# Performance work log

Hardware: AMD Instinct MI355X
Metric: run time of the kernel (lower is better)

The kernel has to match this reference:

```python
import jax, jax.numpy as jnp
import numpy as np

N = 20000      # nodes
E = 640000     # edges
Z = 10         # elements (one-hot node_attrs dim)
H = 128        # hidden channels
B = 32         # graphs in batch
NB = 8         # Bessel basis size
L = 2          # interaction layers
R_MAX = 5.0


def _sph(u):
    # real spherical harmonics, lmax=2 -> 9 components; u: [E,3] unit vectors
    x, y, z = u[:, 0], u[:, 1], u[:, 2]
    c1 = 0.4886025119
    return jnp.stack([
        jnp.full_like(x, 0.2820947918),
        c1 * y, c1 * z, c1 * x,
        1.0925484306 * x * y,
        1.0925484306 * y * z,
        0.3153915653 * (3.0 * z * z - 1.0),
        1.0925484306 * x * z,
        0.5462742153 * (x * x - y * y),
    ], axis=-1)  # [E,9]


def _radial(r):
    # Bessel radial basis with smooth cosine cutoff; r: [E]
    n = jnp.arange(1, NB + 1, dtype=r.dtype)  # [NB]
    pref = jnp.sqrt(2.0 / R_MAX)
    bessel = pref * jnp.sin(n[None, :] * jnp.pi * r[:, None] / R_MAX) / r[:, None]
    env = 0.5 * (jnp.cos(jnp.pi * jnp.minimum(r, R_MAX) / R_MAX) + 1.0)
    env = env * (r < R_MAX).astype(r.dtype)
    return bessel * env[:, None]  # [E,NB]


def setup_inputs() -> dict:
    key = jax.random.key(0)
    ks = jax.random.split(key, 16)
    species = jax.random.randint(ks[0], (N,), 0, Z)
    node_attrs = jax.nn.one_hot(species, Z, dtype=jnp.float32)
    positions = jax.random.normal(ks[1], (N, 3), dtype=jnp.float32) * 3.0
    edge_index = jax.random.randint(ks[2], (2, E), 0, N)
    shifts = jnp.zeros((E, 3), dtype=jnp.float32)
    batch = jnp.sort(jax.random.randint(ks[3], (N,), 0, B))
    s = lambda k, shp, fan: jax.random.normal(k, shp, dtype=jnp.float32) / np.sqrt(fan)
    return dict(
        positions=positions,
        node_attrs=node_attrs,
        shifts=shifts,
        atomic_energies=jax.random.normal(ks[4], (Z,), dtype=jnp.float32),
        W_embed=s(ks[5], (Z, H), Z),
        W_msg=s(ks[6], (L, H, H), H),
        W_rad=s(ks[7], (L, NB, H), NB),
        w_sh=s(ks[8], (L, 9), 9),
        W_prod=s(ks[9], (L, H, H), H),
        W_sc=s(ks[10], (L, H, H), H),
        W_read=s(ks[11], (L, H), H),
        scale=jnp.float32(1.0),
        shift=jnp.float32(0.0),
        edge_index=edge_index,
        batch=batch,
    )


def reference(positions, node_attrs, shifts, atomic_energies, W_embed, W_msg,
              W_rad, w_sh, W_prod, W_sc, W_read, scale, shift,
              edge_index, batch):
    src, dst = edge_index[0], edge_index[1]

    def inter_energy(pos):
        # edge vectors / lengths (get_edge_vectors_and_lengths)
        vec = pos[dst] - pos[src] + shifts          # [E,3]
        r = jnp.sqrt(jnp.sum(vec * vec, -1) + 1e-12)
        sh = _sph(vec / r[:, None])                 # [E,9]
        rad = _radial(r)                            # [E,NB]
        h = node_attrs @ W_embed                    # node_embedding [N,H]
        node_es = jnp.zeros((N,), pos.dtype)        # pair_node_energy zeros
        for l in range(L):
            sc = h @ W_sc[l]                        # self-connection
            # interaction: edge message = gathered feats x weights x radial x angular
            m = (h[src] @ W_msg[l]) * (rad @ W_rad[l]) * (sh @ w_sh[l])[:, None]
            agg = jax.ops.segment_sum(m, dst, num_segments=N)  # scatter_sum -> nodes
            h = jax.nn.silu(agg @ W_prod[l]) + sc   # product + sc
            node_es = node_es + h @ W_read[l]       # readout
        node_inter = scale * node_es + shift        # scale_shift
        inter_e = jax.ops.segment_sum(node_inter, batch, num_segments=B)
        return jnp.sum(inter_e)

    # forces = -dE/dpositions (get_outputs with compute_force=True)
    forces = -jax.grad(inter_energy)(positions)
    return forces
```

## Files before the change

kernel.cpp:

```cpp
#include <hip/hip_runtime.h>
#include <math.h>

#define N_NODES 20000
#define N_EDGES 640000
#define NZ 10
#define HD 128
#define NBESS 8
#define GS 16
#define TPS 132
#define NH (N_NODES*HD)
#define HH (HD*HD)
#define RMAXF 5.0f
#define PI_F 3.14159265358979323846f
#define C_PREF 0.6324555320336759f
#define SH_C0 0.2820947918f
#define SH_C1 0.4886025119f
#define SH_C2 1.0925484306f
#define SH_C6 0.3153915653f
#define SH_C8 0.5462742153f

__device__ __forceinline__ float sigm(float x){ return 1.0f/(1.0f+expf(-x)); }

__global__ void zeroi_k(int* __restrict__ p, int n){
  int i = blockIdx.x*256+threadIdx.x;
  if (i < n) p[i] = 0;
}
__global__ void hist_k(const int* __restrict__ srcI, const int* __restrict__ dstI,
                       int* __restrict__ cd, int* __restrict__ cs){
  int e = blockIdx.x*256+threadIdx.x;
  if (e >= N_EDGES) return;
  atomicAdd(&cd[dstI[e]], 1);
  atomicAdd(&cs[srcI[e]], 1);
}
__global__ void scan_k(const int* __restrict__ cnt2, int* __restrict__ rp2){
  const int* cnt = cnt2 + blockIdx.x*N_NODES;
  int* rp = rp2 + blockIdx.x*(N_NODES+1);
  __shared__ int part[1024];
  int t = threadIdx.x;
  const int CH = (N_NODES+1023)/1024;
  int base = t*CH, s = 0;
  for (int i=0;i<CH;i++){ int j=base+i; if (j<N_NODES) s += cnt[j]; }
  part[t] = s; __syncthreads();
  for (int off=1; off<1024; off<<=1){
    int v = (t>=off) ? part[t-off] : 0;
    __syncthreads();
    part[t] += v;
    __syncthreads();
  }
  int run = (t>0) ? part[t-1] : 0;
  for (int i=0;i<CH;i++){ int j=base+i; if (j<N_NODES){ rp[j]=run; run += cnt[j]; } }
  if (t==1023) rp[N_NODES] = part[1023];
}
__global__ void cpyi_k(const int* __restrict__ a, int* __restrict__ b, int n){
  int i = blockIdx.x*256+threadIdx.x;
  if (i < n) b[i] = a[i];
}
__global__ void csrfill_k(const int* __restrict__ srcI, const int* __restrict__ dstI,
                          int* __restrict__ curd, int* __restrict__ curs,
                          int* __restrict__ pdArr, int2* __restrict__ sdD,
                          int2* __restrict__ pdS){
  int e = blockIdx.x*256+threadIdx.x;
  if (e >= N_EDGES) return;
  int s = srcI[e], d = dstI[e];
  int pd = atomicAdd(&curd[d],1);
  int ps = atomicAdd(&curs[s],1);
  pdArr[e] = pd;
  sdD[pd] = make_int2(s,d);
  pdS[ps] = make_int2(pd,d);
}

__global__ void species_k(const float* __restrict__ attrs, int* __restrict__ spec){
  int n = blockIdx.x*256+threadIdx.x;
  if (n >= N_NODES) return;
  const float* a = attrs + n*NZ;
  int sp = 0;
  #pragma unroll
  for (int z=0; z<NZ; z++) if (a[z] > 0.5f) sp = z;
  spec[n] = sp;
}

__global__ void tables_k(const float* __restrict__ Wemb, const float* __restrict__ Wmsg0,
                         const float* __restrict__ Wsc0,
                         float* __restrict__ T_P0, float* __restrict__ T_sc){
  int z = blockIdx.x, h = threadIdx.x;
  float accP = 0.f, accS = 0.f;
  for (int k=0; k<HD; k++){
    float w = Wemb[z*HD+k];
    accP += w*Wmsg0[k*HD+h];
    accS += w*Wsc0[k*HD+h];
  }
  T_P0[z*HD+h] = accP;
  T_sc[z*HD+h] = accS;
}

__global__ void geom_k(const float* __restrict__ pos, const float* __restrict__ shifts,
                       const int* __restrict__ srcI, const int* __restrict__ dstI,
                       const int* __restrict__ pdArr, const int* __restrict__ spec,
                       const float* __restrict__ wsh, float* __restrict__ geom){
  int e = blockIdx.x*256+threadIdx.x;
  if (e >= N_EDGES) return;
  int s = srcI[e], d = dstI[e];
  float vx = pos[3*d+0]-pos[3*s+0]+shifts[3*e+0];
  float vy = pos[3*d+1]-pos[3*s+1]+shifts[3*e+1];
  float vz = pos[3*d+2]-pos[3*s+2]+shifts[3*e+2];
  float r = sqrtf(vx*vx+vy*vy+vz*vz+1e-12f);
  float inv = 1.0f/r;
  float x = vx*inv, y = vy*inv, z = vz*inv;
  float* g = geom + (size_t)pdArr[e]*GS;
  g[0]=vx; g[1]=vy; g[2]=vz; g[3]=r;
  float theta = PI_F*r/RMAXF;
  float env = (r < RMAXF) ? 0.5f*(cosf(theta)+1.0f) : 0.0f;
  float s1 = sinf(theta), c1 = cosf(theta);
  float sn = s1, cn = c1;
  float pe = C_PREF*inv*env;
  #pragma unroll
  for (int n=0; n<NBESS; n++){
    g[4+n] = pe*sn;
    float sn2 = sn*c1 + cn*s1;
    float cn2 = cn*c1 - sn*s1;
    sn = sn2; cn = cn2;
  }
  float sh[9];
  sh[0] = SH_C0;
  sh[1] = SH_C1*y; sh[2] = SH_C1*z; sh[3] = SH_C1*x;
  sh[4] = SH_C2*x*y; sh[5] = SH_C2*y*z;
  sh[6] = SH_C6*(3.0f*z*z-1.0f);
  sh[7] = SH_C2*x*z; sh[8] = SH_C8*(x*x-y*y);
  float s0v=0.f, s1v=0.f;
  #pragma unroll
  for (int i=0;i<9;i++){ s0v += sh[i]*wsh[i]; s1v += sh[i]*wsh[9+i]; }
  g[12]=s0v; g[13]=s1v; g[14]=__int_as_float(spec[s]); g[15]=0.f;
}

__global__ void transpose_k(const float* __restrict__ Win, float* __restrict__ Wout){
  int i = blockIdx.x*256+threadIdx.x;
  if (i < HH){ int r = i>>7, c = i&127; Wout[c*HD+r] = Win[i]; }
}

__global__ void consts_k(const float* __restrict__ Wread, const float* __restrict__ Wsc,
                         const float* __restrict__ scalep,
                         float* __restrict__ g2vec, float* __restrict__ gh1c){
  int h = threadIdx.x;
  float sc = scalep[0];
  g2vec[h] = sc*Wread[HD+h];
  float acc = Wread[h];
  for (int j=0; j<HD; j++) acc += Wread[HD+j]*Wsc[HH + h*HD + j];
  gh1c[h] = sc*acc;
}

__global__ __launch_bounds__(256,2) void gemm128_k(const float* __restrict__ A,
                                                   const float* __restrict__ W,
                                                   float* __restrict__ out,
                                                   const float* __restrict__ addvec){
  __shared__ __align__(16) float Wl[HH];
  __shared__ __align__(16) float Al[32*HD];
  for (int i=threadIdx.x; i<HH; i+=256) Wl[i] = W[i];
  int row0 = blockIdx.x*32;
  for (int i=threadIdx.x; i<32*HD; i+=256) Al[i] = A[(size_t)row0*HD + i];
  __syncthreads();
  int c4 = (threadIdx.x & 31)*4;
  int rg = (threadIdx.x >> 5)*4;
  float acc[4][4] = {};
  for (int k=0; k<HD; k+=4){
    float4 a0 = *(const float4*)&Al[(rg+0)*HD+k];
    float4 a1 = *(const float4*)&Al[(rg+1)*HD+k];
    float4 a2 = *(const float4*)&Al[(rg+2)*HD+k];
    float4 a3 = *(const float4*)&Al[(rg+3)*HD+k];
    #pragma unroll
    for (int kk=0; kk<4; kk++){
      float4 w = *(const float4*)&Wl[(k+kk)*HD + c4];
      float v0 = (&a0.x)[kk], v1 = (&a1.x)[kk], v2 = (&a2.x)[kk], v3 = (&a3.x)[kk];
      acc[0][0]+=v0*w.x; acc[0][1]+=v0*w.y; acc[0][2]+=v0*w.z; acc[0][3]+=v0*w.w;
      acc[1][0]+=v1*w.x; acc[1][1]+=v1*w.y; acc[1][2]+=v1*w.z; acc[1][3]+=v1*w.w;
      acc[2][0]+=v2*w.x; acc[2][1]+=v2*w.y; acc[2][2]+=v2*w.z; acc[2][3]+=v2*w.w;
      acc[3][0]+=v3*w.x; acc[3][1]+=v3*w.y; acc[3][2]+=v3*w.z; acc[3][3]+=v3*w.w;
    }
  }
  float4 av = make_float4(0.f,0.f,0.f,0.f);
  if (addvec) av = *(const float4*)&addvec[c4];
  #pragma unroll
  for (int rr=0; rr<4; rr++){
    float4 o;
    o.x = acc[rr][0]+av.x; o.y = acc[rr][1]+av.y; o.z = acc[rr][2]+av.z; o.w = acc[rr][3]+av.w;
    *(float4*)&out[(size_t)(row0+rg+rr)*HD + c4] = o;
  }
}

__global__ void h1_k(const float* __restrict__ z, const int* __restrict__ spec,
                     const float* __restrict__ T_sc, float* __restrict__ h){
  int i = blockIdx.x*256+threadIdx.x;
  if (i >= NH) return;
  int n = i>>7, hh = i&127;
  float x = z[i];
  h[i] = x*sigm(x) + T_sc[spec[n]*HD+hh];
}

__global__ void dzb_k(const float* __restrict__ z, const float* __restrict__ gvecc,
                      float* __restrict__ dz){
  int i = blockIdx.x*256+threadIdx.x;
  if (i >= NH) return;
  float x = z[i]; float sg = sigm(x);
  dz[i] = gvecc[i&127]*sg*(1.0f + x*(1.0f-sg));
}

__global__ void dzf_k(const float* __restrict__ z, const float* __restrict__ gh,
                      float* __restrict__ dz){
  int i = blockIdx.x*256+threadIdx.x;
  if (i >= NH) return;
  float x = z[i]; float sg = sigm(x);
  dz[i] = gh[i]*sg*(1.0f + x*(1.0f-sg));
}

__device__ __forceinline__ float dot8(float4 ra, float4 rb, const float* w){
  return ra.x*w[0]+ra.y*w[1]+ra.z*w[2]+ra.w*w[3]+rb.x*w[4]+rb.y*w[5]+rb.z*w[6]+rb.w*w[7];
}

__global__ __launch_bounds__(256) void gatherD0_k(const float* __restrict__ geom,
        const int* __restrict__ rp, const float* __restrict__ T_P0,
        const float* __restrict__ Wrad, float* __restrict__ out){
  __shared__ float tp[NZ*TPS];
  for (int i=threadIdx.x; i<NZ*HD; i+=256){ int z=i>>7, h=i&127; tp[z*TPS+h]=T_P0[i]; }
  __syncthreads();
  int wave = threadIdx.x>>6, lane = threadIdx.x&63;
  int node = blockIdx.x*4 + wave;
  float wv0[NBESS], wv1[NBESS];
  #pragma unroll
  for (int n=0;n<NBESS;n++){ wv0[n]=Wrad[n*HD+lane]; wv1[n]=Wrad[n*HD+64+lane]; }
  int b = rp[node], en = rp[node+1];
  float acc0 = 0.f, acc1 = 0.f;
  for (int i=b; i<en; i++){
    const float* g = geom + (size_t)i*GS;
    float4 ra = *(const float4*)(g+4);
    float4 rb = *(const float4*)(g+8);
    float shs = g[12];
    int sp = __float_as_int(g[14]);
    acc0 += tp[sp*TPS+lane]    * (shs*dot8(ra,rb,wv0));
    acc1 += tp[sp*TPS+64+lane] * (shs*dot8(ra,rb,wv1));
  }
  out[(size_t)node*HD+lane]    = acc0;
  out[(size_t)node*HD+64+lane] = acc1;
}

__global__ __launch_bounds__(256) void gatherD_k(const float* __restrict__ geom,
        const int* __restrict__ rp, const int2* __restrict__ sdD,
        const float* __restrict__ rows,
        const float* __restrict__ Wrad, int shsOff, float* __restrict__ out){
  int wave = threadIdx.x>>6, lane = threadIdx.x&63;
  int node = blockIdx.x*4 + wave;
  float wv0[NBESS], wv1[NBESS];
  #pragma unroll
  for (int n=0;n<NBESS;n++){ wv0[n]=Wrad[n*HD+lane]; wv1[n]=Wrad[n*HD+64+lane]; }
  int b = rp[node], en = rp[node+1];
  float acc0 = 0.f, acc1 = 0.f;
  int i = b;
  for (; i+4 <= en; i+=4){
    int2 t0=sdD[i+0], t1=sdD[i+1], t2=sdD[i+2], t3=sdD[i+3];
    const float* g0=geom+(size_t)(i+0)*GS; const float* g1=geom+(size_t)(i+1)*GS;
    const float* g2=geom+(size_t)(i+2)*GS; const float* g3=geom+(size_t)(i+3)*GS;
    float4 ra0=*(const float4*)(g0+4), rb0=*(const float4*)(g0+8);
    float4 ra1=*(const float4*)(g1+4), rb1=*(const float4*)(g1+8);
    float4 ra2=*(const float4*)(g2+4), rb2=*(const float4*)(g2+8);
    float4 ra3=*(const float4*)(g3+4), rb3=*(const float4*)(g3+8);
    float s0=g0[shsOff], s1=g1[shsOff], s2=g2[shsOff], s3=g3[shsOff];
    float p00=rows[(size_t)t0.x*HD+lane], p01=rows[(size_t)t0.x*HD+64+lane];
    float p10=rows[(size_t)t1.x*HD+lane], p11=rows[(size_t)t1.x*HD+64+lane];
    float p20=rows[(size_t)t2.x*HD+lane], p21=rows[(size_t)t2.x*HD+64+lane];
    float p30=rows[(size_t)t3.x*HD+lane], p31=rows[(size_t)t3.x*HD+64+lane];
    acc0 += p00*(s0*dot8(ra0,rb0,wv0));  acc1 += p01*(s0*dot8(ra0,rb0,wv1));
    acc0 += p10*(s1*dot8(ra1,rb1,wv0));  acc1 += p11*(s1*dot8(ra1,rb1,wv1));
    acc0 += p20*(s2*dot8(ra2,rb2,wv0));  acc1 += p21*(s2*dot8(ra2,rb2,wv1));
    acc0 += p30*(s3*dot8(ra3,rb3,wv0));  acc1 += p31*(s3*dot8(ra3,rb3,wv1));
  }
  for (; i<en; i++){
    int2 t = sdD[i];
    const float* g = geom + (size_t)i*GS;
    float4 ra = *(const float4*)(g+4);
    float4 rb = *(const float4*)(g+8);
    float shs = g[shsOff];
    acc0 += rows[(size_t)t.x*HD+lane]    * (shs*dot8(ra,rb,wv0));
    acc1 += rows[(size_t)t.x*HD+64+lane] * (shs*dot8(ra,rb,wv1));
  }
  out[(size_t)node*HD+lane]    = acc0;
  out[(size_t)node*HD+64+lane] = acc1;
}

__global__ __launch_bounds__(256) void gatherS_k(const float* __restrict__ geom,
        const int* __restrict__ rp, const int2* __restrict__ pdS,
        const float* __restrict__ rows,
        const float* __restrict__ Wrad, int shsOff, float* __restrict__ out){
  int wave = threadIdx.x>>6, lane = threadIdx.x&63;
  int node = blockIdx.x*4 + wave;
  float wv0[NBESS], wv1[NBESS];
  #pragma unroll
  for (int n=0;n<NBESS;n++){ wv0[n]=Wrad[n*HD+lane]; wv1[n]=Wrad[n*HD+64+lane]; }
  int b = rp[node], en = rp[node+1];
  float acc0 = 0.f, acc1 = 0.f;
  int i = b;
  for (; i+4 <= en; i+=4){
    int2 t0=pdS[i+0], t1=pdS[i+1], t2=pdS[i+2], t3=pdS[i+3];
    const float* g0=geom+(size_t)t0.x*GS; const float* g1=geom+(size_t)t1.x*GS;
    const float* g2=geom+(size_t)t2.x*GS; const float* g3=geom+(size_t)t3.x*GS;
    float4 ra0=*(const float4*)(g0+4), rb0=*(const float4*)(g0+8);
    float4 ra1=*(const float4*)(g1+4), rb1=*(const float4*)(g1+8);
    float4 ra2=*(const float4*)(g2+4), rb2=*(const float4*)(g2+8);
    float4 ra3=*(const float4*)(g3+4), rb3=*(const float4*)(g3+8);
    float s0=g0[shsOff], s1=g1[shsOff], s2=g2[shsOff], s3=g3[shsOff];
    float p00=rows[(size_t)t0.y*HD+lane], p01=rows[(size_t)t0.y*HD+64+lane];
    float p10=rows[(size_t)t1.y*HD+lane], p11=rows[(size_t)t1.y*HD+64+lane];
    float p20=rows[(size_t)t2.y*HD+lane], p21=rows[(size_t)t2.y*HD+64+lane];
    float p30=rows[(size_t)t3.y*HD+lane], p31=rows[(size_t)t3.y*HD+64+lane];
    acc0 += p00*(s0*dot8(ra0,rb0,wv0));  acc1 += p01*(s0*dot8(ra0,rb0,wv1));
    acc0 += p10*(s1*dot8(ra1,rb1,wv0));  acc1 += p11*(s1*dot8(ra1,rb1,wv1));
    acc0 += p20*(s2*dot8(ra2,rb2,wv0));  acc1 += p21*(s2*dot8(ra2,rb2,wv1));
    acc0 += p30*(s3*dot8(ra3,rb3,wv0));  acc1 += p31*(s3*dot8(ra3,rb3,wv1));
  }
  for (; i<en; i++){
    int2 t = pdS[i];
    const float* g = geom + (size_t)t.x*GS;
    float4 ra = *(const float4*)(g+4);
    float4 rb = *(const float4*)(g+8);
    float shs = g[shsOff];
    acc0 += rows[(size_t)t.y*HD+lane]    * (shs*dot8(ra,rb,wv0));
    acc1 += rows[(size_t)t.y*HD+64+lane] * (shs*dot8(ra,rb,wv1));
  }
  out[(size_t)node*HD+lane]    = acc0;
  out[(size_t)node*HD+64+lane] = acc1;
}

__global__ __launch_bounds__(256) void qdotF_k(const float* __restrict__ geom,
        const int2* __restrict__ sdD,
        const float* __restrict__ G1, const float* __restrict__ P1,
        const float* __restrict__ G0, const float* __restrict__ T_P0,
        const float* __restrict__ Wrad, const float* __restrict__ wshp,
        float* __restrict__ gvec){
  __shared__ float wr0[NBESS*HD];
  __shared__ float wr1[NBESS*HD];
  __shared__ float tp0[NZ*TPS];
  __shared__ float ws[18];
  for (int i=threadIdx.x; i<NBESS*HD; i+=256){ wr0[i]=Wrad[i]; wr1[i]=Wrad[NBESS*HD+i]; }
  for (int i=threadIdx.x; i<NZ*HD; i+=256){ int z=i>>7, h=i&127; tp0[z*TPS+h]=T_P0[i]; }
  if (threadIdx.x < 18) ws[threadIdx.x] = wshp[threadIdx.x];
  __syncthreads();
  int i = blockIdx.x*256+threadIdx.x;
  int2 sd = sdD[i];
  int s = sd.x, d = sd.y;
  const float* g = geom + (size_t)i*GS;
  int sp = __float_as_int(g[14]);
  const float4* G1r = (const float4*)(G1 + (size_t)d*HD);
  const float4* P1r = (const float4*)(P1 + (size_t)s*HD);
  const float4* G0r = (const float4*)(G0 + (size_t)d*HD);
  const float* P0l = tp0 + sp*TPS;
  float gr80[NBESS] = {0,0,0,0,0,0,0,0};
  float gr81[NBESS] = {0,0,0,0,0,0,0,0};
  #pragma unroll 2
  for (int k=0; k<32; k++){
    float4 g1q = G1r[k], p1q = P1r[k];
    float4 g0q = G0r[k];
    float4 p0q = *(const float4*)&P0l[4*k];
    float a0 = g1q.x*p1q.x, a1 = g1q.y*p1q.y, a2 = g1q.z*p1q.z, a3 = g1q.w*p1q.w;
    float b0 = g0q.x*p0q.x, b1 = g0q.y*p0q.y, b2 = g0q.z*p0q.z, b3 = g0q.w*p0q.w;
    #pragma unroll
    for (int n=0; n<NBESS; n++){
      const float4 w1 = *(const float4*)&wr1[n*HD + 4*k];
      const float4 w0 = *(const float4*)&wr0[n*HD + 4*k];
      gr81[n] += a0*w1.x + a1*w1.y + a2*w1.z + a3*w1.w;
      gr80[n] += b0*w0.x + b1*w0.y + b2*w0.z + b3*w0.w;
    }
  }
  float vx=g[0], vy=g[1], vz=g[2], r=g[3];
  float shs0 = g[12], shs1 = g[13];
  float gshs0 = 0.f, gshs1 = 0.f;
  float grd[NBESS];
  #pragma unroll
  for (int n=0; n<NBESS; n++){
    float rn = g[4+n];
    gshs0 += rn*gr80[n];
    gshs1 += rn*gr81[n];
    grd[n] = shs0*gr80[n] + shs1*gr81[n];
  }
  float inv = 1.0f/r;
  float x = vx*inv, y = vy*inv, z = vz*inv;
  float gs1=gshs0*ws[1]+gshs1*ws[10], gs2=gshs0*ws[2]+gshs1*ws[11];
  float gs3=gshs0*ws[3]+gshs1*ws[12], gs4=gshs0*ws[4]+gshs1*ws[13];
  float gs5=gshs0*ws[5]+gshs1*ws[14], gs6=gshs0*ws[6]+gshs1*ws[15];
  float gs7=gshs0*ws[7]+gshs1*ws[16], gs8=gshs0*ws[8]+gshs1*ws[17];
  float gux = SH_C1*gs3 + SH_C2*(y*gs4 + z*gs7) + 1.0925484306f*x*gs8;
  float guy = SH_C1*gs1 + SH_C2*(x*gs4 + z*gs5) - 1.0925484306f*y*gs8;
  float guz = SH_C1*gs2 + SH_C2*(y*gs5 + x*gs7) + 1.8923493918f*z*gs6;
  float udot = x*gux + y*guy + z*guz;
  float gr = 0.f;
  if (r < RMAXF){
    float theta = PI_F*r/RMAXF;
    float s1 = sinf(theta), c1 = cosf(theta);
    float env  = 0.5f*(c1+1.0f);
    float denv = -0.5f*(PI_F/RMAXF)*s1;
    float sn = s1, cn = c1;
    #pragma unroll
    for (int n=0; n<NBESS; n++){
      float an = (float)(n+1)*(PI_F/RMAXF);
      float bess  = C_PREF*sn*inv;
      float dbess = C_PREF*inv*(an*cn - sn*inv);
      gr += grd[n]*(dbess*env + bess*denv);
      float sn2 = sn*c1 + cn*s1;
      float cn2 = cn*c1 - sn*s1;
      sn = sn2; cn = cn2;
    }
  }
  gvec[3*(size_t)i+0] = gr*x + (gux - x*udot)*inv;
  gvec[3*(size_t)i+1] = gr*y + (guy - y*udot)*inv;
  gvec[3*(size_t)i+2] = gr*z + (guz - z*udot)*inv;
}

__global__ __launch_bounds__(256) void fgather_k(const int* __restrict__ rpd,
        const int* __restrict__ rps, const int2* __restrict__ pdS,
        const float* __restrict__ gvec, float* __restrict__ F){
  int wave = threadIdx.x>>6, lane = threadIdx.x&63;
  int n = blockIdx.x*4 + wave;
  float fx=0.f, fy=0.f, fz=0.f;
  int b=rps[n], en=rps[n+1];
  for (int i=b+lane; i<en; i+=64){ int j=pdS[i].x; fx+=gvec[3*(size_t)j]; fy+=gvec[3*(size_t)j+1]; fz+=gvec[3*(size_t)j+2]; }
  b=rpd[n]; en=rpd[n+1];
  for (int i=b+lane; i<en; i+=64){ fx-=gvec[3*(size_t)i]; fy-=gvec[3*(size_t)i+1]; fz-=gvec[3*(size_t)i+2]; }
  #pragma unroll
  for (int off=1; off<64; off<<=1){
    fx += __shfl_xor(fx, off);
    fy += __shfl_xor(fy, off);
    fz += __shfl_xor(fz, off);
  }
  if (lane==0){ F[3*(size_t)n]=fx; F[3*(size_t)n+1]=fy; F[3*(size_t)n+2]=fz; }
}

extern "C" void kernel_launch(void* const* d_in, const int* in_sizes, int n_in,
                              void* d_out, int out_size, void* d_ws, size_t ws_size,
                              hipStream_t stream){
  const float* pos    = (const float*)d_in[0];
  const float* attrs  = (const float*)d_in[1];
  const float* shifts = (const float*)d_in[2];
  const float* Wemb   = (const float*)d_in[4];
  const float* Wmsg   = (const float*)d_in[5];
  const float* Wrad   = (const float*)d_in[6];
  const float* wsh    = (const float*)d_in[7];
  const float* Wprod  = (const float*)d_in[8];
  const float* Wsc    = (const float*)d_in[9];
  const float* Wread  = (const float*)d_in[10];
  const float* scalep = (const float*)d_in[11];
  const int*   eidx   = (const int*)d_in[13];
  const int* srcI = eidx;
  const int* dstI = eidx + N_EDGES;
  float* F = (float*)d_out;
  (void)ws_size; (void)in_sizes; (void)n_in; (void)out_size;

  float* w = (float*)d_ws;
  size_t off = 0;
  auto alloc = [&](size_t nf){ float* p = w + off; off += nf; return p; };
  float* geom = alloc((size_t)N_EDGES*GS);
  float* h1   = alloc(NH);
  float* P1   = alloc(NH);
  float* z0   = alloc(NH);
  float* z1   = alloc(NH);
  float* Svar = alloc(NH);
  float* agg  = alloc(NH);
  float* Gbuf1= alloc(NH);
  float* Gbuf0= alloc(NH);
  float* A1   = alloc(NH);
  float* gh1  = alloc(NH);
  float* WT0  = alloc(HH);
  float* WT1  = alloc(HH);
  float* WT2  = alloc(HH);
  float* T_P0 = alloc(NZ*HD);
  float* T_sc = alloc(NZ*HD);
  float* g2vec = alloc(HD);
  float* gh1c  = alloc(HD);
  float* gvec  = alloc((size_t)N_EDGES*3);
  int* ibase = (int*)(w + off);
  int* cnt2 = ibase;
  int* rp2  = ibase + 2*N_NODES;
  int* cur2 = rp2 + 2*(N_NODES+1);
  int* pdArr= cur2 + 2*(N_NODES+1);
  int* spec = pdArr + N_EDGES;
  int2* sdD = (int2*)(((size_t)(spec + N_NODES) + 7) & ~(size_t)7);
  int2* pdS = sdD + N_EDGES;
  int* rpd = rp2;
  int* rps = rp2 + (N_NODES+1);
  int* curd = cur2;
  int* curs = cur2 + (N_NODES+1);

  const int GEMM_GRID = N_NODES/32;
  const int NODE_GRID = N_NODES/4;
  const int E_GRID    = N_EDGES/256;

  zeroi_k<<<(2*N_NODES+255)/256, 256, 0, stream>>>(cnt2, 2*N_NODES);
  hist_k<<<E_GRID, 256, 0, stream>>>(srcI, dstI, cnt2, cnt2+N_NODES);
  scan_k<<<2, 1024, 0, stream>>>(cnt2, rp2);
  cpyi_k<<<(2*(N_NODES+1)+255)/256, 256, 0, stream>>>(rp2, cur2, 2*(N_NODES+1));
  csrfill_k<<<E_GRID, 256, 0, stream>>>(srcI, dstI, curd, curs, pdArr, sdD, pdS);

  species_k<<<(N_NODES+255)/256, 256, 0, stream>>>(attrs, spec);
  geom_k<<<E_GRID, 256, 0, stream>>>(pos, shifts, srcI, dstI, pdArr, spec, wsh, geom);
  tables_k<<<NZ, HD, 0, stream>>>(Wemb, Wmsg, Wsc, T_P0, T_sc);
  transpose_k<<<HH/256, 256, 0, stream>>>(Wprod+HH, WT0);
  transpose_k<<<HH/256, 256, 0, stream>>>(Wprod,    WT1);
  transpose_k<<<HH/256, 256, 0, stream>>>(Wmsg+HH,  WT2);
  consts_k<<<1, HD, 0, stream>>>(Wread, Wsc, scalep, g2vec, gh1c);

  gatherD0_k<<<NODE_GRID, 256, 0, stream>>>(geom, rpd, T_P0, Wrad, agg);
  gemm128_k<<<GEMM_GRID, 256, 0, stream>>>(agg, Wprod, z0, nullptr);
  h1_k<<<NH/256, 256, 0, stream>>>(z0, spec, T_sc, h1);

  gemm128_k<<<GEMM_GRID, 256, 0, stream>>>(h1, Wmsg+HH, P1, nullptr);
  gatherD_k<<<NODE_GRID, 256, 0, stream>>>(geom, rpd, sdD, P1, Wrad+NBESS*HD, 13, agg);
  gemm128_k<<<GEMM_GRID, 256, 0, stream>>>(agg, Wprod+HH, z1, nullptr);

  dzb_k<<<NH/256, 256, 0, stream>>>(z1, g2vec, Svar);
  gemm128_k<<<GEMM_GRID, 256, 0, stream>>>(Svar, WT0, Gbuf1, nullptr);
  gatherS_k<<<NODE_GRID, 256, 0, stream>>>(geom, rps, pdS, Gbuf1, Wrad+NBESS*HD, 13, A1);
  gemm128_k<<<GEMM_GRID, 256, 0, stream>>>(A1, WT2, gh1, gh1c);
  dzf_k<<<NH/256, 256, 0, stream>>>(z0, gh1, Svar);
  gemm128_k<<<GEMM_GRID, 256, 0, stream>>>(Svar, WT1, Gbuf0, nullptr);
  qdotF_k<<<E_GRID, 256, 0, stream>>>(geom, sdD, Gbuf1, P1, Gbuf0, T_P0, Wrad, wsh, gvec);
  fgather_k<<<NODE_GRID, 256, 0, stream>>>(rpd, rps, pdS, gvec, F);
}
```

Baseline: 678.0 us.

## Replace FP32 node GEMMs with split-bf16 MFMA GEMMs

Replaces the shared-memory FP32 128x128 GEMM with an MFMA kernel that splits each FP32 operand into bf16 hi and lo parts and accumulates three products, which keeps accuracy close to FP32. Weights are pre-split and stored in both transposed and non-transposed layouts by one prep kernel, replacing the three transpose kernels. The aim is to cut the FP32 ALU cost of the six node GEMMs. In exchange, A is converted in-register on every call, B is read straight from global memory without LDS staging, and the output stores are strided by column.

```diff
diff --git a/kernel.cpp b/kernel.cpp
--- a/kernel.cpp
+++ b/kernel.cpp
@@ -19,7 +19,16 @@
 #define SH_C6 0.3153915653f
 #define SH_C8 0.5462742153f
 
+typedef __attribute__((ext_vector_type(8))) short short8v;
+typedef __attribute__((ext_vector_type(4))) float f32x4;
+
 __device__ __forceinline__ float sigm(float x){ return 1.0f/(1.0f+expf(-x)); }
+__device__ __forceinline__ unsigned short bf16r(float f){
+  unsigned int u = __float_as_uint(f);
+  unsigned int r = (u + 0x7fffu + ((u>>16)&1u))>>16;
+  return (unsigned short)r;
+}
+__device__ __forceinline__ float bf2f(unsigned short h){ return __uint_as_float(((unsigned int)h)<<16); }
 
 __global__ void zeroi_k(int* __restrict__ p, int n){
   int i = blockIdx.x*256+threadIdx.x;
@@ -91,6 +100,22 @@
   }
   T_P0[z*HD+h] = accP;
   T_sc[z*HD+h] = accS;
+}
+
+__global__ void wprep_k(const float* __restrict__ Wprod, const float* __restrict__ Wmsg,
+                        unsigned short* __restrict__ Wb){
+  int i = blockIdx.x*256+threadIdx.x;
+  if (i >= 3*HH) return;
+  int m = i/HH, r = i%HH;
+  int k = r>>7, n = r&127;
+  const float* src = (m==0) ? Wprod : (m==1) ? (Wprod+HH) : (Wmsg+HH);
+  float f = src[r];
+  unsigned short hi = bf16r(f);
+  unsigned short lo = bf16r(f - bf2f(hi));
+  Wb[((m*2+1)*2+0)*HH + r] = hi;
+  Wb[((m*2+1)*2+1)*HH + r] = lo;
+  Wb[((m*2+0)*2+0)*HH + n*HD + k] = hi;
+  Wb[((m*2+0)*2+1)*HH + n*HD + k] = lo;
 }
 
 __global__ void geom_k(const float* __restrict__ pos, const float* __restrict__ shifts,
@@ -132,11 +157,6 @@
   g[12]=s0v; g[13]=s1v; g[14]=__int_as_float(spec[s]); g[15]=0.f;
 }
 
-__global__ void transpose_k(const float* __restrict__ Win, float* __restrict__ Wout){
-  int i = blockIdx.x*256+threadIdx.x;
-  if (i < HH){ int r = i>>7, c = i&127; Wout[c*HD+r] = Win[i]; }
-}
-
 __global__ void consts_k(const float* __restrict__ Wread, const float* __restrict__ Wsc,
                          const float* __restrict__ scalep,
                          float* __restrict__ g2vec, float* __restrict__ gh1c){
@@ -148,41 +168,47 @@
   gh1c[h] = sc*acc;
 }
 
-__global__ __launch_bounds__(256,2) void gemm128_k(const float* __restrict__ A,
-                                                   const float* __restrict__ W,
-                                                   float* __restrict__ out,
-                                                   const float* __restrict__ addvec){
-  __shared__ __align__(16) float Wl[HH];
-  __shared__ __align__(16) float Al[32*HD];
-  for (int i=threadIdx.x; i<HH; i+=256) Wl[i] = W[i];
-  int row0 = blockIdx.x*32;
-  for (int i=threadIdx.x; i<32*HD; i+=256) Al[i] = A[(size_t)row0*HD + i];
-  __syncthreads();
-  int c4 = (threadIdx.x & 31)*4;
-  int rg = (threadIdx.x >> 5)*4;
-  float acc[4][4] = {};
-  for (int k=0; k<HD; k+=4){
-    float4 a0 = *(const float4*)&Al[(rg+0)*HD+k];
-    float4 a1 = *(const float4*)&Al[(rg+1)*HD+k];
-    float4 a2 = *(const float4*)&Al[(rg+2)*HD+k];
-    float4 a3 = *(const float4*)&Al[(rg+3)*HD+k];
+__global__ __launch_bounds__(256) void gemmM_k(const float* __restrict__ A,
+        const unsigned short* __restrict__ BThi, const unsigned short* __restrict__ BTlo,
+        float* __restrict__ C, const float* __restrict__ addvec){
+  int w = threadIdx.x>>6, l = threadIdx.x&63;
+  int row0 = blockIdx.x*32 + (w&1)*16;
+  int col0 = (w>>1)*64;
+  int lrow = l&15, lk8 = (l>>4)*8;
+  f32x4 acc[4];
+  #pragma unroll
+  for (int t=0;t<4;t++) acc[t] = (f32x4){0.f,0.f,0.f,0.f};
+  for (int ks=0; ks<4; ks++){
+    const float* ap = A + (size_t)(row0+lrow)*HD + ks*32 + lk8;
+    float4 a01 = *(const float4*)ap;
+    float4 a23 = *(const float4*)(ap+4);
+    float av[8] = {a01.x,a01.y,a01.z,a01.w,a23.x,a23.y,a23.z,a23.w};
+    short8v ahi, alo;
     #pragma unroll
-    for (int kk=0; kk<4; kk++){
-      float4 w = *(const float4*)&Wl[(k+kk)*HD + c4];
-      float v0 = (&a0.x)[kk], v1 = (&a1.x)[kk], v2 = (&a2.x)[kk], v3 = (&a3.x)[kk];
-      acc[0][0]+=v0*w.x; acc[0][1]+=v0*w.y; acc[0][2]+=v0*w.z; acc[0][3]+=v0*w.w;
-      acc[1][0]+=v1*w.x; acc[1][1]+=v1*w.y; acc[1][2]+=v1*w.z; acc[1][3]+=v1*w.w;
-      acc[2][0]+=v2*w.x; acc[2][1]+=v2*w.y; acc[2][2]+=v2*w.z; acc[2][3]+=v2*w.w;
-      acc[3][0]+=v3*w.x; acc[3][1]+=v3*w.y; acc[3][2]+=v3*w.z; acc[3][3]+=v3*w.w;
+    for (int j=0;j<8;j++){
+      unsigned short hb = bf16r(av[j]);
+      ahi[j] = (short)hb;
+      alo[j] = (short)bf16r(av[j] - bf2f(hb));
     }
-  }
-  float4 av = make_float4(0.f,0.f,0.f,0.f);
-  if (addvec) av = *(const float4*)&addvec[c4];
-  #pragma unroll
-  for (int rr=0; rr<4; rr++){
-    float4 o;
-    o.x = acc[rr][0]+av.x; o.y = acc[rr][1]+av.y; o.z = acc[rr][2]+av.z; o.w = acc[rr][3]+av.w;
-    *(float4*)&out[(size_t)(row0+rg+rr)*HD + c4] = o;
+    #pragma unroll
+    for (int t=0;t<4;t++){
+      size_t boff = (size_t)(col0 + t*16 + lrow)*HD + ks*32 + lk8;
+      short8v bhi = *(const short8v*)(BThi + boff);
+      short8v blo = *(const short8v*)(BTlo + boff);
+      acc[t] = __builtin_amdgcn_mfma_f32_16x16x32_bf16(ahi, bhi, acc[t], 0,0,0);
+      acc[t] = __builtin_amdgcn_mfma_f32_16x16x32_bf16(ahi, blo, acc[t], 0,0,0);
+      acc[t] = __builtin_amdgcn_mfma_f32_16x16x32_bf16(alo, bhi, acc[t], 0,0,0);
+    }
+  }
+  #pragma unroll
+  for (int t=0;t<4;t++){
+    int col = col0 + t*16 + lrow;
+    float av = addvec ? addvec[col] : 0.f;
+    #pragma unroll
+    for (int r=0;r<4;r++){
+      int rr = row0 + (l>>4)*4 + r;
+      C[(size_t)rr*HD + col] = acc[t][r] + av;
+    }
   }
 }
 
@@ -464,14 +490,12 @@
   float* Gbuf0= alloc(NH);
   float* A1   = alloc(NH);
   float* gh1  = alloc(NH);
-  float* WT0  = alloc(HH);
-  float* WT1  = alloc(HH);
-  float* WT2  = alloc(HH);
   float* T_P0 = alloc(NZ*HD);
   float* T_sc = alloc(NZ*HD);
   float* g2vec = alloc(HD);
   float* gh1c  = alloc(HD);
   float* gvec  = alloc((size_t)N_EDGES*3);
+  unsigned short* Wb = (unsigned short*)alloc(6*HH);
   int* ibase = (int*)(w + off);
   int* cnt2 = ibase;
   int* rp2  = ibase + 2*N_NODES;
@@ -485,6 +509,13 @@
   int* curd = cur2;
   int* curs = cur2 + (N_NODES+1);
 
+  const unsigned short* Wp0T_h = Wb + 0*HH; const unsigned short* Wp0T_l = Wb + 1*HH;
+  const unsigned short* Wp0R_h = Wb + 2*HH; const unsigned short* Wp0R_l = Wb + 3*HH;
+  const unsigned short* Wp1T_h = Wb + 4*HH; const unsigned short* Wp1T_l = Wb + 5*HH;
+  const unsigned short* Wp1R_h = Wb + 6*HH; const unsigned short* Wp1R_l = Wb + 7*HH;
+  const unsigned short* Wm1T_h = Wb + 8*HH; const unsigned short* Wm1T_l = Wb + 9*HH;
+  const unsigned short* Wm1R_h = Wb +10*HH; const unsigned short* Wm1R_l = Wb +11*HH;
+
   const int GEMM_GRID = N_NODES/32;
   const int NODE_GRID = N_NODES/4;
   const int E_GRID    = N_EDGES/256;
@@ -498,25 +529,23 @@
   species_k<<<(N_NODES+255)/256, 256, 0, stream>>>(attrs, spec);
   geom_k<<<E_GRID, 256, 0, stream>>>(pos, shifts, srcI, dstI, pdArr, spec, wsh, geom);
   tables_k<<<NZ, HD, 0, stream>>>(Wemb, Wmsg, Wsc, T_P0, T_sc);
-  transpose_k<<<HH/256, 256, 0, stream>>>(Wprod+HH, WT0);
-  transpose_k<<<HH/256, 256, 0, stream>>>(Wprod,    WT1);
-  transpose_k<<<HH/256, 256, 0, stream>>>(Wmsg+HH,  WT2);
+  wprep_k<<<(3*HH+255)/256, 256, 0, stream>>>(Wprod, Wmsg, (unsigned short*)Wb);
   consts_k<<<1, HD, 0, stream>>>(Wread, Wsc, scalep, g2vec, gh1c);
 
   gatherD0_k<<<NODE_GRID, 256, 0, stream>>>(geom, rpd, T_P0, Wrad, agg);
-  gemm128_k<<<GEMM_GRID, 256, 0, stream>>>(agg, Wprod, z0, nullptr);
+  gemmM_k<<<GEMM_GRID, 256, 0, stream>>>(agg, Wp0T_h, Wp0T_l, z0, nullptr);
   h1_k<<<NH/256, 256, 0, stream>>>(z0, spec, T_sc, h1);
 
-  gemm128_k<<<GEMM_GRID, 256, 0, stream>>>(h1, Wmsg+HH, P1, nullptr);
+  gemmM_k<<<GEMM_GRID, 256, 0, stream>>>(h1, Wm1T_h, Wm1T_l, P1, nullptr);
   gatherD_k<<<NODE_GRID, 256, 0, stream>>>(geom, rpd, sdD, P1, Wrad+NBESS*HD, 13, agg);
-  gemm128_k<<<GEMM_GRID, 256, 0, stream>>>(agg, Wprod+HH, z1, nullptr);
+  gemmM_k<<<GEMM_GRID, 256, 0, stream>>>(agg, Wp1T_h, Wp1T_l, z1, nullptr);
 
   dzb_k<<<NH/256, 256, 0, stream>>>(z1, g2vec, Svar);
-  gemm128_k<<<GEMM_GRID, 256, 0, stream>>>(Svar, WT0, Gbuf1, nullptr);
+  gemmM_k<<<GEMM_GRID, 256, 0, stream>>>(Svar, Wp1R_h, Wp1R_l, Gbuf1, nullptr);
   gatherS_k<<<NODE_GRID, 256, 0, stream>>>(geom, rps, pdS, Gbuf1, Wrad+NBESS*HD, 13, A1);
-  gemm128_k<<<GEMM_GRID, 256, 0, stream>>>(A1, WT2, gh1, gh1c);
+  gemmM_k<<<GEMM_GRID, 256, 0, stream>>>(A1, Wm1R_h, Wm1R_l, gh1, gh1c);
   dzf_k<<<NH/256, 256, 0, stream>>>(z0, gh1, Svar);
-  gemm128_k<<<GEMM_GRID, 256, 0, stream>>>(Svar, WT1, Gbuf0, nullptr);
+  gemmM_k<<<GEMM_GRID, 256, 0, stream>>>(Svar, Wp0R_h, Wp0R_l, Gbuf0, nullptr);
   qdotF_k<<<E_GRID, 256, 0, stream>>>(geom, sdD, Gbuf1, P1, Gbuf0, T_P0, Wrad, wsh, gvec);
   fgather_k<<<NODE_GRID, 256, 0, stream>>>(rpd, rps, pdS, gvec, F);
 }
```

Result: faster. 663.0 us (-2.2%).
